# Optimization experiments

Hardware: AMD Instinct MI355X
Metric: run time of the kernel (lower is better)

The kernel has to match this reference:

```python
import jax, jax.numpy as jnp
import numpy as np

K = 20           # top_k
EPS_NORM = 1e-12  # F.normalize default eps


def setup_inputs() -> dict:
    key = jax.random.key(0)
    ks = jax.random.split(key, 16)
    B, C, R, S, SCB, ST, H = 8192, 3755, 214, 13, 30, 6, 64
    return {
        "char_logits": jax.random.normal(ks[0], (B, C), jnp.float32),
        "radical_logits": jax.random.normal(ks[1], (B, R), jnp.float32),
        "structure": jax.random.normal(ks[2], (B, S), jnp.float32),
        "stroke_count": jax.random.normal(ks[3], (B, SCB), jnp.float32),
        "stroke_types": jax.random.normal(ks[4], (B, ST), jnp.float32),
        "radical_mask": jax.random.randint(ks[5], (C, R), 0, 2, jnp.int32),
        "structure_label": jax.random.randint(ks[6], (C,), 0, S, jnp.int32),
        "stroke_count_label": jax.random.randint(ks[7], (C,), 0, SCB, jnp.int32),
        "stroke_type_sig": jax.random.uniform(ks[8], (C, ST), jnp.float32),
        "W1": jax.random.normal(ks[9], (6, H), jnp.float32) * 0.3,
        "b1": jax.random.normal(ks[10], (H,), jnp.float32) * 0.1,
        "W2": jax.random.normal(ks[11], (H, 1), jnp.float32) * 0.3,
        "b2": jax.random.normal(ks[12], (1,), jnp.float32) * 0.1,
        "reranker_weight": jnp.asarray(0.1, jnp.float32),
    }


def _features(char_logits, radical_logits, structure, stroke_count, stroke_types,
              radical_mask, structure_label, stroke_count_label, stroke_type_sig,
              top_idx):
    sg = jax.lax.stop_gradient
    # all model outputs except char_logits are detached by caller; char_logits
    # is detached inside _compute_features for the neural-confidence feature
    rl, st, sc, sty = sg(radical_logits), sg(structure), sg(stroke_count), sg(stroke_types)
    cl_d = sg(char_logits)

    # feature 1/2: radical match & false-alarm ratios
    radical_probs = jax.nn.sigmoid(rl)                              # (B, R)
    cand_mask = radical_mask[top_idx].astype(jnp.float32)           # (B, K, R)
    detected = jnp.einsum('br,bkr->bk', radical_probs, cand_mask)   # (B, K)
    cand_counts = jnp.maximum(cand_mask.sum(-1), 1.0)
    radical_match_ratio = detected / cand_counts
    total_prob = jnp.maximum(radical_probs.sum(-1, keepdims=True), 1e-6)  # (B,1)
    false_alarm_mass = radical_probs.sum(-1, keepdims=True) - detected
    radical_false_ratio = false_alarm_mass / total_prob

    # feature 3: structure match probability
    structure_probs = jax.nn.softmax(st, axis=-1)                   # (B, S)
    cand_structure = structure_label[top_idx]                       # (B, K)
    structure_match = jnp.take_along_axis(structure_probs, cand_structure, axis=1)

    # feature 4: normalized stroke-count distance
    stroke_pred = jnp.argmax(sc, axis=-1)                           # (B,)
    cand_stroke = stroke_count_label[top_idx]                       # (B, K)
    stroke_distance = jnp.abs(stroke_pred[:, None] - cand_stroke).astype(jnp.float32) / 29.0

    # feature 5: zero-masked stroke-type cosine
    cand_sig = stroke_type_sig[top_idx]                             # (B, K, 6)
    sig_norm_val = jnp.linalg.norm(cand_sig, axis=-1)               # (B, K)
    has_sig = (sig_norm_val > 1e-6).astype(jnp.float32)
    pred_norm = sty / jnp.maximum(jnp.linalg.norm(sty, axis=-1, keepdims=True), EPS_NORM)
    cand_adj = cand_sig + 1e-8 * (1.0 - has_sig)[..., None]
    cand_norm = cand_adj / jnp.maximum(jnp.linalg.norm(cand_adj, axis=-1, keepdims=True), EPS_NORM)
    stroke_type_cos = jnp.einsum('bd,bkd->bk', pred_norm, cand_norm) * has_sig

    # feature 6: detached neural confidence
    neural_probs = jax.nn.softmax(cl_d, axis=-1)                    # (B, C)
    neural_conf = jnp.take_along_axis(neural_probs, top_idx, axis=1)

    return jnp.stack([radical_match_ratio, radical_false_ratio, structure_match,
                      stroke_distance, stroke_type_cos, neural_conf], axis=-1)  # (B, K, 6)


def reference(char_logits, radical_logits, structure, stroke_count, stroke_types,
              radical_mask, structure_label, stroke_count_label, stroke_type_sig,
              W1, b1, W2, b2, reranker_weight):
    B = char_logits.shape[0]
    top_logits, top_idx = jax.lax.top_k(char_logits, K)             # (B, K)
    feats = _features(char_logits, radical_logits, structure, stroke_count,
                      stroke_types, radical_mask, structure_label,
                      stroke_count_label, stroke_type_sig, top_idx)
    h = jax.nn.relu(feats @ W1 + b1)                                # (B, K, H)
    rerank_scores = (h @ W2 + b2)[..., 0]                           # (B, K)
    combined_top = top_logits + reranker_weight * rerank_scores
    rows = jnp.arange(B)[:, None]
    return char_logits.at[rows, top_idx].set(combined_top)
```

## Files before the change

### kernel.cpp

```cpp
#include <hip/hip_runtime.h>
#include <math.h>

#define NB   8192
#define NC   3755
#define NR   214
#define NS   13
#define NSC  30
#define NST  6
#define NH   64
#define KTOP 20
#define NT   256
#define EPT  15

__global__ __launch_bounds__(NT) void reranker_kernel(
    const float* __restrict__ char_logits,
    const float* __restrict__ radical_logits,
    const float* __restrict__ structure,
    const float* __restrict__ stroke_count,
    const float* __restrict__ stroke_types,
    const int*   __restrict__ radical_mask,
    const int*   __restrict__ structure_label,
    const int*   __restrict__ stroke_count_label,
    const float* __restrict__ stroke_type_sig,
    const float* __restrict__ W1,
    const float* __restrict__ b1,
    const float* __restrict__ W2,
    const float* __restrict__ b2,
    const float* __restrict__ rw,
    float*       __restrict__ out)
{
    const int b    = blockIdx.x;
    const int tid  = threadIdx.x;
    const int lane = tid & 63;
    const int wave = tid >> 6;

    __shared__ float s_rv[4];
    __shared__ int   s_ri[4];
    __shared__ float s_red8[8];
    __shared__ float s_topval[KTOP];
    __shared__ int   s_topidx[KTOP];
    __shared__ float s_probs[NR];
    __shared__ float s_struct[NS];
    __shared__ float s_pred[NST];
    __shared__ float s_feats[KTOP][6];
    __shared__ float s_misc[4];

    const size_t rowOff = (size_t)b * NC;

    float v[EPT];
#pragma unroll
    for (int t = 0; t < EPT; ++t) {
        int idx = tid + t * NT;
        float x = -INFINITY;
        if (idx < NC) {
            x = char_logits[rowOff + idx];
            out[rowOff + idx] = x;
        }
        v[t] = x;
    }

    float lv = -INFINITY; int li = NC;
#pragma unroll
    for (int t = 0; t < EPT; ++t) {
        int idx = tid + t * NT;
        if (v[t] > lv) { lv = v[t]; li = idx; }
    }

    for (int k = 0; k < KTOP; ++k) {
        float rv = lv; int ri = li;
#pragma unroll
        for (int off = 32; off > 0; off >>= 1) {
            float ov = __shfl_down(rv, off);
            int   oi = __shfl_down(ri, off);
            if (ov > rv || (ov == rv && oi < ri)) { rv = ov; ri = oi; }
        }
        if (lane == 0) { s_rv[wave] = rv; s_ri[wave] = ri; }
        __syncthreads();
        if (tid == 0) {
            float bv = s_rv[0]; int bi = s_ri[0];
#pragma unroll
            for (int w = 1; w < 4; ++w) {
                float ov = s_rv[w]; int oi = s_ri[w];
                if (ov > bv || (ov == bv && oi < bi)) { bv = ov; bi = oi; }
            }
            s_topval[k] = bv; s_topidx[k] = bi;
        }
        __syncthreads();
        int sel = s_topidx[k];
        if ((sel & (NT - 1)) == tid) {
            int t = sel >> 8;
            v[t] = -INFINITY;
            lv = -INFINITY; li = NC;
#pragma unroll
            for (int tt = 0; tt < EPT; ++tt) {
                int idx = tid + tt * NT;
                if (v[tt] > lv) { lv = v[tt]; li = idx; }
            }
        }
    }

    const float rowmax = s_topval[0];

    float le = 0.f;
#pragma unroll
    for (int t = 0; t < EPT; ++t) le += expf(v[t] - rowmax);
#pragma unroll
    for (int off = 32; off > 0; off >>= 1) le += __shfl_down(le, off);

    float p = 0.f;
    if (tid < NR) {
        float x = radical_logits[(size_t)b * NR + tid];
        p = 1.f / (1.f + expf(-x));
        s_probs[tid] = p;
    }
#pragma unroll
    for (int off = 32; off > 0; off >>= 1) p += __shfl_down(p, off);

    if (lane == 0) { s_red8[wave] = le; s_red8[4 + wave] = p; }
    __syncthreads();

    if (tid == 0) {
        float s = s_red8[0] + s_red8[1] + s_red8[2] + s_red8[3];
        float extra = 0.f;
#pragma unroll
        for (int k = 0; k < KTOP; ++k) extra += expf(s_topval[k] - rowmax);
        s_misc[0] = s + extra;
        s_misc[1] = s_red8[4] + s_red8[5] + s_red8[6] + s_red8[7];
    } else if (tid == 64) {
        float sv[NS]; float m = -INFINITY;
#pragma unroll
        for (int i = 0; i < NS; ++i) { sv[i] = structure[(size_t)b * NS + i]; m = fmaxf(m, sv[i]); }
        float s = 0.f;
#pragma unroll
        for (int i = 0; i < NS; ++i) { sv[i] = expf(sv[i] - m); s += sv[i]; }
        float inv = 1.f / s;
#pragma unroll
        for (int i = 0; i < NS; ++i) s_struct[i] = sv[i] * inv;
    } else if (tid == 128) {
        float bv = -INFINITY; int bi = 0;
#pragma unroll
        for (int i = 0; i < NSC; ++i) {
            float x = stroke_count[(size_t)b * NSC + i];
            if (x > bv) { bv = x; bi = i; }
        }
        s_misc[2] = (float)bi;
    } else if (tid == 192) {
        float t6[NST]; float ss = 0.f;
#pragma unroll
        for (int i = 0; i < NST; ++i) { t6[i] = stroke_types[(size_t)b * NST + i]; ss += t6[i] * t6[i]; }
        float inv = 1.f / fmaxf(sqrtf(ss), 1e-12f);
#pragma unroll
        for (int i = 0; i < NST; ++i) s_pred[i] = t6[i] * inv;
    }
    __syncthreads();

    const float sumexp = s_misc[0];
    const float total  = s_misc[1];
    const float spred  = s_misc[2];

    for (int k = wave; k < KTOP; k += 4) {
        int ci = s_topidx[k];
        const int* mrow = radical_mask + (size_t)ci * NR;
        float det = 0.f, cnt = 0.f;
        for (int r = lane; r < NR; r += 64) {
            float m = (float)mrow[r];
            det += s_probs[r] * m;
            cnt += m;
        }
#pragma unroll
        for (int off = 32; off > 0; off >>= 1) {
            det += __shfl_down(det, off);
            cnt += __shfl_down(cnt, off);
        }
        if (lane == 0) {
            float f1 = det / fmaxf(cnt, 1.f);
            float f2 = (total - det) / fmaxf(total, 1e-6f);
            float f3 = s_struct[structure_label[ci]];
            float f4 = fabsf(spred - (float)stroke_count_label[ci]) * (1.f / 29.f);
            float sig[NST]; float ss = 0.f;
#pragma unroll
            for (int i = 0; i < NST; ++i) { sig[i] = stroke_type_sig[(size_t)ci * NST + i]; ss += sig[i] * sig[i]; }
            float nrm = sqrtf(ss);
            float has = (nrm > 1e-6f) ? 1.f : 0.f;
            float add = 1e-8f * (1.f - has);
            float ss2 = 0.f;
#pragma unroll
            for (int i = 0; i < NST; ++i) { sig[i] += add; ss2 += sig[i] * sig[i]; }
            float inv = 1.f / fmaxf(sqrtf(ss2), 1e-12f);
            float dot = 0.f;
#pragma unroll
            for (int i = 0; i < NST; ++i) dot += s_pred[i] * sig[i] * inv;
            float f5 = dot * has;
            float f6 = expf(s_topval[k] - rowmax) / sumexp;
            s_feats[k][0] = f1; s_feats[k][1] = f2; s_feats[k][2] = f3;
            s_feats[k][3] = f4; s_feats[k][4] = f5; s_feats[k][5] = f6;
        }
    }
    __syncthreads();

    const float w = rw[0];
    for (int k = wave; k < KTOP; k += 4) {
        float f0 = s_feats[k][0], f1 = s_feats[k][1], f2 = s_feats[k][2];
        float f3 = s_feats[k][3], f4 = s_feats[k][4], f5 = s_feats[k][5];
        float acc = b1[lane];
        acc += f0 * W1[0 * NH + lane];
        acc += f1 * W1[1 * NH + lane];
        acc += f2 * W1[2 * NH + lane];
        acc += f3 * W1[3 * NH + lane];
        acc += f4 * W1[4 * NH + lane];
        acc += f5 * W1[5 * NH + lane];
        float h = fmaxf(acc, 0.f);
        float part = h * W2[lane];
#pragma unroll
        for (int off = 32; off > 0; off >>= 1) part += __shfl_down(part, off);
        if (lane == 0) {
            float score = part + b2[0];
            out[rowOff + s_topidx[k]] = s_topval[k] + w * score;
        }
    }
}

extern "C" void kernel_launch(void* const* d_in, const int* in_sizes, int n_in,
                              void* d_out, int out_size, void* d_ws, size_t ws_size,
                              hipStream_t stream) {
    (void)in_sizes; (void)n_in; (void)out_size; (void)d_ws; (void)ws_size;
    const float* char_logits        = (const float*)d_in[0];
    const float* radical_logits     = (const float*)d_in[1];
    const float* structure          = (const float*)d_in[2];
    const float* stroke_count       = (const float*)d_in[3];
    const float* stroke_types       = (const float*)d_in[4];
    const int*   radical_mask       = (const int*)d_in[5];
    const int*   structure_label    = (const int*)d_in[6];
    const int*   stroke_count_label = (const int*)d_in[7];
    const float* stroke_type_sig    = (const float*)d_in[8];
    const float* W1                 = (const float*)d_in[9];
    const float* b1                 = (const float*)d_in[10];
    const float* W2                 = (const float*)d_in[11];
    const float* b2                 = (const float*)d_in[12];
    const float* rw                 = (const float*)d_in[13];
    float* out = (float*)d_out;

    reranker_kernel<<<NB, NT, 0, stream>>>(
        char_logits, radical_logits, structure, stroke_count, stroke_types,
        radical_mask, structure_label, stroke_count_label, stroke_type_sig,
        W1, b1, W2, b2, rw, out);
}
```

Measured before the change: 421.6 us.

## Run per-wave top-k independently and merge wave lists in one thread

Each of the four waves now extracts its own top-20 candidates with xor-shuffle reductions and no block barriers, recording them in shared memory. A single thread then does a 4-way merge to form the global top-20. The softmax correction term now covers all 80 per-wave extracted values, since each was masked out of that wave's register values. This removes the two __syncthreads per top-k iteration, at the cost of every lane rescanning its 15 registers each iteration and a serial merge in one thread.

```diff
diff --git a/kernel.cpp b/kernel.cpp
--- a/kernel.cpp
+++ b/kernel.cpp
@@ -34,15 +34,15 @@
     const int lane = tid & 63;
     const int wave = tid >> 6;
 
-    __shared__ float s_rv[4];
-    __shared__ int   s_ri[4];
-    __shared__ float s_red8[8];
+    __shared__ float s_wval[4][KTOP];
+    __shared__ int   s_widx[4][KTOP];
     __shared__ float s_topval[KTOP];
     __shared__ int   s_topidx[KTOP];
     __shared__ float s_probs[NR];
     __shared__ float s_struct[NS];
     __shared__ float s_pred[NST];
     __shared__ float s_feats[KTOP][6];
+    __shared__ float s_red8[8];
     __shared__ float s_misc[4];
 
     const size_t rowOff = (size_t)b * NC;
@@ -59,45 +59,65 @@
         v[t] = x;
     }
 
-    float lv = -INFINITY; int li = NC;
+    float lv = -INFINITY; int li = 0x7fffffff;
 #pragma unroll
     for (int t = 0; t < EPT; ++t) {
-        int idx = tid + t * NT;
-        if (v[t] > lv) { lv = v[t]; li = idx; }
+        if (v[t] > lv) { lv = v[t]; li = tid + t * NT; }
     }
 
     for (int k = 0; k < KTOP; ++k) {
         float rv = lv; int ri = li;
 #pragma unroll
-        for (int off = 32; off > 0; off >>= 1) {
-            float ov = __shfl_down(rv, off);
-            int   oi = __shfl_down(ri, off);
+        for (int off = 1; off < 64; off <<= 1) {
+            float ov = __shfl_xor(rv, off);
+            int   oi = __shfl_xor(ri, off);
             if (ov > rv || (ov == rv && oi < ri)) { rv = ov; ri = oi; }
         }
-        if (lane == 0) { s_rv[wave] = rv; s_ri[wave] = ri; }
-        __syncthreads();
-        if (tid == 0) {
-            float bv = s_rv[0]; int bi = s_ri[0];
-#pragma unroll
-            for (int w = 1; w < 4; ++w) {
-                float ov = s_rv[w]; int oi = s_ri[w];
-                if (ov > bv || (ov == bv && oi < bi)) { bv = ov; bi = oi; }
+        if (lane == 0) { s_wval[wave][k] = rv; s_widx[wave][k] = ri; }
+#pragma unroll
+        for (int tt = 0; tt < EPT; ++tt) {
+            if (tid + tt * NT == ri) v[tt] = -INFINITY;
+        }
+        lv = -INFINITY; li = 0x7fffffff;
+#pragma unroll
+        for (int tt = 0; tt < EPT; ++tt) {
+            if (v[tt] > lv) { lv = v[tt]; li = tid + tt * NT; }
+        }
+    }
+    __syncthreads();
+
+    if (tid == 0) {
+        int p0 = 0, p1 = 0, p2 = 0, p3 = 0;
+        for (int k = 0; k < KTOP; ++k) {
+            float bv = -INFINITY; int bi = 0x7fffffff; int bw = 0;
+            {
+                float vv = (p0 < KTOP) ? s_wval[0][p0] : -INFINITY;
+                int   ii = (p0 < KTOP) ? s_widx[0][p0] : 0x7fffffff;
+                if (vv > bv || (vv == bv && ii < bi)) { bv = vv; bi = ii; bw = 0; }
+            }
+            {
+                float vv = (p1 < KTOP) ? s_wval[1][p1] : -INFINITY;
+                int   ii = (p1 < KTOP) ? s_widx[1][p1] : 0x7fffffff;
+                if (vv > bv || (vv == bv && ii < bi)) { bv = vv; bi = ii; bw = 1; }
+            }
+            {
+                float vv = (p2 < KTOP) ? s_wval[2][p2] : -INFINITY;
+                int   ii = (p2 < KTOP) ? s_widx[2][p2] : 0x7fffffff;
+                if (vv > bv || (vv == bv && ii < bi)) { bv = vv; bi = ii; bw = 2; }
+            }
+            {
+                float vv = (p3 < KTOP) ? s_wval[3][p3] : -INFINITY;
+                int   ii = (p3 < KTOP) ? s_widx[3][p3] : 0x7fffffff;
+                if (vv > bv || (vv == bv && ii < bi)) { bv = vv; bi = ii; bw = 3; }
             }
             s_topval[k] = bv; s_topidx[k] = bi;
-        }
-        __syncthreads();
-        int sel = s_topidx[k];
-        if ((sel & (NT - 1)) == tid) {
-            int t = sel >> 8;
-            v[t] = -INFINITY;
-            lv = -INFINITY; li = NC;
-#pragma unroll
-            for (int tt = 0; tt < EPT; ++tt) {
-                int idx = tid + tt * NT;
-                if (v[tt] > lv) { lv = v[tt]; li = idx; }
-            }
-        }
-    }
+            if      (bw == 0) p0++;
+            else if (bw == 1) p1++;
+            else if (bw == 2) p2++;
+            else              p3++;
+        }
+    }
+    __syncthreads();
 
     const float rowmax = s_topval[0];
 
@@ -123,7 +143,9 @@
         float s = s_red8[0] + s_red8[1] + s_red8[2] + s_red8[3];
         float extra = 0.f;
 #pragma unroll
-        for (int k = 0; k < KTOP; ++k) extra += expf(s_topval[k] - rowmax);
+        for (int w = 0; w < 4; ++w)
+#pragma unroll
+            for (int k = 0; k < KTOP; ++k) extra += expf(s_wval[w][k] - rowmax);
         s_misc[0] = s + extra;
         s_misc[1] = s_red8[4] + s_red8[5] + s_red8[6] + s_red8[7];
     } else if (tid == 64) {
```

Result: slower. 478.4 us (+13.5%).
